# Performance work log

Hardware: AMD Instinct MI355X
Metric: run time of the kernel (lower is better)

Reference implementation:

```python
import jax, jax.numpy as jnp
import numpy as np

B, E, S = 4, 128, 4096


def setup_inputs() -> dict:
    key = jax.random.key(0)
    ks = jax.random.split(key, 7)
    x = jax.random.normal(ks[0], (B, E, S), dtype=jnp.float32)
    sd = 1.0 / np.sqrt(E)
    Wq = jax.random.normal(ks[1], (E, E), dtype=jnp.float32) * sd
    bq = jax.random.normal(ks[2], (E,), dtype=jnp.float32) * sd
    Wk = jax.random.normal(ks[3], (E, E), dtype=jnp.float32) * sd
    bk = jax.random.normal(ks[4], (E,), dtype=jnp.float32) * sd
    Wv = jax.random.normal(ks[5], (E, E), dtype=jnp.float32) * sd
    bv = jax.random.normal(ks[6], (E,), dtype=jnp.float32) * sd
    return {"x": x, "Wq": Wq, "bq": bq, "Wk": Wk, "bk": bk, "Wv": Wv, "bv": bv}


def reference(x, Wq, bq, Wk, bk, Wv, bv):
    # x: [B, E, S] -> [B, S, E] (matches x.transpose(1, 2) in the source)
    xt = jnp.swapaxes(x, 1, 2)
    # torch nn.Linear convention: y = x @ W.T + b
    q = xt @ Wq.T + bq  # [B, S, E]
    k = xt @ Wk.T + bk  # [B, S, E]
    v = xt @ Wv.T + bv  # [B, S, E]
    scale = 1.0 / jnp.sqrt(jnp.asarray(q.shape[-1], q.dtype))
    # full score matrix [B, S, S] -> softmax -> weighted sum of V
    scores = jax.nn.softmax(jnp.einsum("bse,bte->bst", q, k) * scale, axis=-1)
    out = jnp.einsum("bst,bte->bse", scores, v)  # [B, S, E]
    return out
```

## Files before the change

### kernel.cpp

```cpp
#include <hip/hip_runtime.h>

#define B_ 4
#define E_ 128
#define S_ 4096

typedef _Float16 half8 __attribute__((ext_vector_type(8)));
typedef _Float16 half4v __attribute__((ext_vector_type(4)));
typedef float floatx4 __attribute__((ext_vector_type(4)));

#define KQS (0.088388347648318447f * 1.4426950408889634f)

__device__ __forceinline__ floatx4 mfma16(half8 a, half8 b, floatx4 c) {
    return __builtin_amdgcn_mfma_f32_16x16x32_f16(a, b, c, 0, 0, 0);
}

__device__ __forceinline__ void gl_lds16(const void* g, void* l) {
    __builtin_amdgcn_global_load_lds(
        (const __attribute__((address_space(1))) void*)g,
        (__attribute__((address_space(3))) void*)l, 16, 0, 0);
}

__global__ void prep_w(const float* __restrict__ Wq, const float* __restrict__ Wk,
                       const float* __restrict__ Wv, _Float16* __restrict__ Wh) {
    int i = blockIdx.x * 256 + threadIdx.x;
    int mat = i >> 14;
    int j = i & 16383;
    float v = (mat == 0) ? Wq[j] * KQS : ((mat == 1) ? Wk[j] : Wv[j]);
    Wh[i] = (_Float16)v;
}

__global__ __launch_bounds__(256, 2) void proj(
    const float* __restrict__ x, const _Float16* __restrict__ Wh,
    const float* __restrict__ bq, const float* __restrict__ bk, const float* __restrict__ bv,
    _Float16* __restrict__ Qh, _Float16* __restrict__ Kh, _Float16* __restrict__ Vt) {
    __shared__ __align__(16) _Float16 sx[64 * 136];
    __shared__ __align__(16) _Float16 sk[64 * 136];
    __shared__ __align__(16) _Float16 sv[128 * 72];

    const int bid = blockIdx.x;
    const int b = bid >> 6;
    const int s0 = (bid & 63) << 6;
    const int tid = threadIdx.x;
    const int w = tid >> 6, lane = tid & 63;
    const int c = lane & 15, q = lane >> 4;

    const float* xb = x + (size_t)b * E_ * S_;
#pragma unroll
    for (int k = 0; k < 32; ++k) {
        int idx = k * 256 + tid;
        int e = idx >> 6, s = idx & 63;
        sx[s * 136 + e] = (_Float16)xb[e * S_ + s0 + s];
    }
    __syncthreads();

    half8 xf[4];
#pragma unroll
    for (int ch = 0; ch < 4; ++ch)
        xf[ch] = *(const half8*)&sx[(w * 16 + c) * 136 + ch * 32 + q * 8];
    __syncthreads();

    for (int eot = 0; eot < 8; ++eot) {
        half8 wf[3][4];
#pragma unroll
        for (int m = 0; m < 3; ++m)
#pragma unroll
            for (int ch = 0; ch < 4; ++ch)
                wf[m][ch] = *(const half8*)(Wh + ((m * E_ + eot * 16 + c) * E_ + ch * 32 + q * 8));

        floatx4 aq, ak, av;
        float bqv = bq[eot * 16 + c] * KQS;
        float bkv = bk[eot * 16 + c];
#pragma unroll
        for (int i = 0; i < 4; ++i) {
            aq[i] = bqv; ak[i] = bkv; av[i] = bv[eot * 16 + q * 4 + i];
        }
#pragma unroll
        for (int ch = 0; ch < 4; ++ch) {
            aq = mfma16(xf[ch], wf[0][ch], aq);
            ak = mfma16(xf[ch], wf[1][ch], ak);
            av = mfma16(wf[2][ch], xf[ch], av);
        }
#pragma unroll
        for (int i = 0; i < 4; ++i) {
            sx[(w * 16 + q * 4 + i) * 136 + eot * 16 + c] = (_Float16)aq[i];
            sk[(w * 16 + q * 4 + i) * 136 + eot * 16 + c] = (_Float16)ak[i];
            sv[(eot * 16 + q * 4 + i) * 72 + w * 16 + c] = (_Float16)av[i];
        }
    }
    __syncthreads();

#pragma unroll
    for (int p = 0; p < 4; ++p) {
        int idx = p * 256 + tid;
        int row = idx >> 4, chk = idx & 15;
        *(half8*)(Qh + ((size_t)(b * S_) + s0 + row) * E_ + chk * 8) =
            *(const half8*)&sx[row * 136 + chk * 8];
        *(half8*)(Kh + ((size_t)(b * S_) + s0 + row) * E_ + chk * 8) =
            *(const half8*)&sk[row * 136 + chk * 8];
        int vrow = idx >> 3, vch = idx & 7;
        *(half8*)(Vt + ((size_t)b * E_ + vrow) * S_ + s0 + vch * 8) =
            *(const half8*)&sv[vrow * 72 + vch * 8];
    }
}

__global__ __launch_bounds__(256, 2) void flash_attn(
    const _Float16* __restrict__ Qh, const _Float16* __restrict__ Kh,
    const _Float16* __restrict__ Vt, _Float16* __restrict__ Opart,
    float* __restrict__ lsum) {
    __shared__ __align__(16) _Float16 smem[32768];

    const int bid = blockIdx.x;
    const int b = bid >> 7, rem = bid & 127, qt = rem >> 2, part = rem & 3;
    const int tid = threadIdx.x, w = tid >> 6, lane = tid & 63;
    const int c = lane & 15, q = lane >> 4;

    const _Float16* Kb = Kh + ((size_t)b * S_ + part * 1024) * E_;
    const _Float16* Vb = Vt + (size_t)b * E_ * S_ + part * 1024;

    half8 qf[2][4];
    {
        const _Float16* Qb = Qh + ((size_t)b * S_ + qt * 128 + w * 32 + c) * E_;
#pragma unroll
        for (int st = 0; st < 2; ++st)
#pragma unroll
            for (int ch = 0; ch < 4; ++ch)
                qf[st][ch] = *(const half8*)(Qb + st * 16 * E_ + ch * 32 + q * 8);
    }

    floatx4 o[2][8];
    float lacc[2] = {0.f, 0.f};
#pragma unroll
    for (int st = 0; st < 2; ++st)
#pragma unroll
        for (int et = 0; et < 8; ++et) o[st][et] = (floatx4){0.f, 0.f, 0.f, 0.f};

    auto stageK = [&](int kt, int bi) {
        _Float16* Kd = smem + bi * 8192;
#pragma unroll
        for (int r = 0; r < 4; ++r) {
            int row = w * 16 + r * 4 + q;
            int lb = c ^ (row & 15);
            gl_lds16(Kb + ((size_t)(kt * 64 + row)) * E_ + lb * 8, Kd + (w * 16 + r * 4) * E_);
        }
    };
    auto stageV = [&](int kt, int bi) {
        _Float16* Vd = smem + 16384 + bi * 8192;
#pragma unroll
        for (int r = 0; r < 4; ++r) {
            int row = w * 32 + r * 8 + (lane >> 3);
            int lb = (lane & 7) ^ (row & 7);
            gl_lds16(Vb + (size_t)row * S_ + kt * 64 + lb * 8, Vd + (w * 32 + r * 8) * 64);
        }
    };

    stageK(0, 0); stageV(0, 0);
    for (int kt = 0; kt < 16; ++kt) {
        __syncthreads();
        if (kt + 1 < 16) { stageK(kt + 1, (kt + 1) & 1); stageV(kt + 1, (kt + 1) & 1); }

        const _Float16* K0 = smem + (kt & 1) * 8192;
        const _Float16* V0 = smem + 16384 + (kt & 1) * 8192;

        floatx4 sa[2][4];
#pragma unroll
        for (int st = 0; st < 2; ++st)
#pragma unroll
            for (int nt = 0; nt < 4; ++nt) sa[st][nt] = (floatx4){0.f, 0.f, 0.f, 0.f};
#pragma unroll
        for (int nt = 0; nt < 4; ++nt) {
            int row = nt * 16 + c;
#pragma unroll
            for (int ch = 0; ch < 4; ++ch) {
                int blk = (ch * 4 + q) ^ (row & 15);
                half8 kf = *(const half8*)(K0 + row * E_ + blk * 8);
                sa[0][nt] = mfma16(kf, qf[0][ch], sa[0][nt]);
                sa[1][nt] = mfma16(kf, qf[1][ch], sa[1][nt]);
            }
        }

        half8 pf[2][2];
#pragma unroll
        for (int st = 0; st < 2; ++st) {
#pragma unroll
            for (int nt = 0; nt < 4; ++nt) {
#pragma unroll
                for (int i = 0; i < 4; ++i) sa[st][nt][i] = exp2f(sa[st][nt][i]);
                lacc[st] += (sa[st][nt][0] + sa[st][nt][1]) + (sa[st][nt][2] + sa[st][nt][3]);
            }
#pragma unroll
            for (int ch = 0; ch < 2; ++ch) {
                half8 f;
#pragma unroll
                for (int j = 0; j < 8; ++j)
                    f[j] = (_Float16)sa[st][ch * 2 + (j >> 2)][j & 3];
                pf[st][ch] = f;
            }
        }

#pragma unroll
        for (int et = 0; et < 8; ++et) {
            int e = et * 16 + c;
            int sw = e & 7;
#pragma unroll
            for (int ch = 0; ch < 2; ++ch) {
                half4v lo = *(const half4v*)(V0 + e * 64 + (((ch * 4 + (q >> 1)) ^ sw) << 3) + (q & 1) * 4);
                half4v hi = *(const half4v*)(V0 + e * 64 + (((ch * 4 + 2 + (q >> 1)) ^ sw) << 3) + (q & 1) * 4);
                half8 vf = {lo[0], lo[1], lo[2], lo[3], hi[0], hi[1], hi[2], hi[3]};
                o[0][et] = mfma16(pf[0][ch], vf, o[0][et]);
                o[1][et] = mfma16(pf[1][ch], vf, o[1][et]);
            }
        }
    }
    __syncthreads();

#pragma unroll
    for (int st = 0; st < 2; ++st) {
        lacc[st] += __shfl_xor(lacc[st], 16);
        lacc[st] += __shfl_xor(lacc[st], 32);
    }
    if (q == 0) {
#pragma unroll
        for (int st = 0; st < 2; ++st)
            lsum[(size_t)bid * 128 + w * 32 + st * 16 + c] = lacc[st];
    }

    _Float16* Ot = smem + w * (32 * 136);
#pragma unroll
    for (int st = 0; st < 2; ++st) {
        float linv[4];
#pragma unroll
        for (int i = 0; i < 4; ++i) linv[i] = 1.0f / __shfl(lacc[st], q * 4 + i);
#pragma unroll
        for (int et = 0; et < 8; ++et)
#pragma unroll
            for (int i = 0; i < 4; ++i)
                Ot[(st * 16 + q * 4 + i) * 136 + et * 16 + c] = (_Float16)(o[st][et][i] * linv[i]);
    }
    __syncthreads();
    _Float16* OG = Opart + (size_t)bid * 16384;
#pragma unroll
    for (int p = 0; p < 8; ++p) {
        int idx = p * 64 + lane;
        int row = idx >> 4, chk = idx & 15;
        *(half8*)(OG + (w * 32 + row) * 128 + chk * 8) = *(const half8*)(Ot + row * 136 + chk * 8);
    }
}

__global__ void combine(const _Float16* __restrict__ Opart, const float* __restrict__ lsum,
                        float* __restrict__ out) {
    int t = blockIdx.x * 256 + threadIdx.x;
    int e4 = t & 31;
    int row = t >> 5;
    int b = row >> 12, s = row & 4095;
    int qt = s >> 7, r = s & 127;
    int bid0 = b * 128 + qt * 4;

    float l0 = lsum[(size_t)(bid0 + 0) * 128 + r];
    float l1 = lsum[(size_t)(bid0 + 1) * 128 + r];
    float l2 = lsum[(size_t)(bid0 + 2) * 128 + r];
    float l3 = lsum[(size_t)(bid0 + 3) * 128 + r];
    float inv = 1.f / (l0 + l1 + l2 + l3);
    float w0 = l0 * inv, w1 = l1 * inv, w2 = l2 * inv, w3 = l3 * inv;

    half4v n0 = *(const half4v*)(Opart + (size_t)(bid0 + 0) * 16384 + r * 128 + e4 * 4);
    half4v n1 = *(const half4v*)(Opart + (size_t)(bid0 + 1) * 16384 + r * 128 + e4 * 4);
    half4v n2 = *(const half4v*)(Opart + (size_t)(bid0 + 2) * 16384 + r * 128 + e4 * 4);
    half4v n3 = *(const half4v*)(Opart + (size_t)(bid0 + 3) * 16384 + r * 128 + e4 * 4);
    floatx4 res;
#pragma unroll
    for (int j = 0; j < 4; ++j)
        res[j] = (float)n0[j] * w0 + (float)n1[j] * w1 + (float)n2[j] * w2 + (float)n3[j] * w3;
    *(floatx4*)(out + (size_t)row * 128 + e4 * 4) = res;
}

extern "C" void kernel_launch(void* const* d_in, const int* in_sizes, int n_in,
                              void* d_out, int out_size, void* d_ws, size_t ws_size,
                              hipStream_t stream) {
    const float* x  = (const float*)d_in[0];
    const float* Wq = (const float*)d_in[1];
    const float* bq = (const float*)d_in[2];
    const float* Wk = (const float*)d_in[3];
    const float* bk = (const float*)d_in[4];
    const float* Wv = (const float*)d_in[5];
    const float* bv = (const float*)d_in[6];
    float* out = (float*)d_out;

    char* p = (char*)d_ws;
    _Float16* Wh = (_Float16*)p;
    _Float16* Qh = (_Float16*)(p + (1 << 17));
    _Float16* Kh = (_Float16*)(p + (1 << 17) + (1 << 22));
    _Float16* Vt = (_Float16*)(p + (1 << 17) + (2 << 22));
    _Float16* Op = (_Float16*)(p + (1 << 17) + (3 << 22));
    float* lsp   = (float*)(p + (1 << 17) + (3 << 22) + (1 << 24));

    prep_w<<<192, 256, 0, stream>>>(Wq, Wk, Wv, Wh);
    proj<<<256, 256, 0, stream>>>(x, Wh, bq, bk, bv, Qh, Kh, Vt);
    flash_attn<<<512, 256, 0, stream>>>(Qh, Kh, Vt, Op, lsp);
    combine<<<2048, 256, 0, stream>>>(Op, lsp, out);
}
```

Before: 141.8 us.

## Switch attention to 32x32x16 MFMA with 256-row query tiles and 8-way KV split

Rewrites the flash attention kernel to use 32x32x16 MFMA tiles, with each wave handling 64 query rows over a 512-key split (8 parts instead of 4). The projection kernel permutes V columns so the P fragments from the 32x32 accumulator layout line up with the V operand. Exp2 and fp16 packing move to raw builtins (exp2 and packed round-toward-zero convert). The aim is higher MFMA throughput and fewer LDS reads per flop, paid for with larger partial outputs, more combine traffic and higher register pressure.

```diff
diff --git a/kernel.cpp b/kernel.cpp
--- a/kernel.cpp
+++ b/kernel.cpp
@@ -6,12 +6,17 @@
 
 typedef _Float16 half8 __attribute__((ext_vector_type(8)));
 typedef _Float16 half4v __attribute__((ext_vector_type(4)));
+typedef __fp16 fp16x2 __attribute__((ext_vector_type(2)));
 typedef float floatx4 __attribute__((ext_vector_type(4)));
+typedef float floatx16 __attribute__((ext_vector_type(16)));
 
 #define KQS (0.088388347648318447f * 1.4426950408889634f)
 
 __device__ __forceinline__ floatx4 mfma16(half8 a, half8 b, floatx4 c) {
     return __builtin_amdgcn_mfma_f32_16x16x32_f16(a, b, c, 0, 0, 0);
+}
+__device__ __forceinline__ floatx16 mfma32(half8 a, half8 b, floatx16 c) {
+    return __builtin_amdgcn_mfma_f32_32x32x16_f16(a, b, c, 0, 0, 0);
 }
 
 __device__ __forceinline__ void gl_lds16(const void* g, void* l) {
@@ -43,6 +48,7 @@
     const int tid = threadIdx.x;
     const int w = tid >> 6, lane = tid & 63;
     const int c = lane & 15, q = lane >> 4;
+    const int pc = (c & 3) | (((c >> 3) & 1) << 2) | (((c >> 2) & 1) << 3);
 
     const float* xb = x + (size_t)b * E_ * S_;
 #pragma unroll
@@ -84,7 +90,7 @@
         for (int i = 0; i < 4; ++i) {
             sx[(w * 16 + q * 4 + i) * 136 + eot * 16 + c] = (_Float16)aq[i];
             sk[(w * 16 + q * 4 + i) * 136 + eot * 16 + c] = (_Float16)ak[i];
-            sv[(eot * 16 + q * 4 + i) * 72 + w * 16 + c] = (_Float16)av[i];
+            sv[(eot * 16 + q * 4 + i) * 72 + w * 16 + pc] = (_Float16)av[i];
         }
     }
     __syncthreads();
@@ -110,167 +116,161 @@
     __shared__ __align__(16) _Float16 smem[32768];
 
     const int bid = blockIdx.x;
-    const int b = bid >> 7, rem = bid & 127, qt = rem >> 2, part = rem & 3;
-    const int tid = threadIdx.x, w = tid >> 6, lane = tid & 63;
-    const int c = lane & 15, q = lane >> 4;
-
-    const _Float16* Kb = Kh + ((size_t)b * S_ + part * 1024) * E_;
-    const _Float16* Vb = Vt + (size_t)b * E_ * S_ + part * 1024;
-
-    half8 qf[2][4];
+    const int b = bid >> 7, rem = bid & 127, qt = rem >> 3, part = rem & 7;
+    const int tid = threadIdx.x, w = tid >> 6, l = tid & 63;
+    const int e5 = l & 31, hi = l >> 5;
+    const int c3 = (l >> 1) & 7;
+    const int c2 = (l >> 1) & 3;
+    const int b0 = (hi ^ l) & 1;
+
+    const _Float16* Kb = Kh + ((size_t)b * S_ + part * 512) * E_;
+    const _Float16* Vb = Vt + (size_t)b * E_ * S_ + part * 512;
+
+    half8 qf[2][8];
     {
-        const _Float16* Qb = Qh + ((size_t)b * S_ + qt * 128 + w * 32 + c) * E_;
-#pragma unroll
-        for (int st = 0; st < 2; ++st)
-#pragma unroll
-            for (int ch = 0; ch < 4; ++ch)
-                qf[st][ch] = *(const half8*)(Qb + st * 16 * E_ + ch * 32 + q * 8);
-    }
-
-    floatx4 o[2][8];
+        const _Float16* Qbase = Qh + ((size_t)b * S_ + qt * 256 + w * 64) * E_;
+#pragma unroll
+        for (int qb = 0; qb < 2; ++qb)
+#pragma unroll
+            for (int ech = 0; ech < 8; ++ech)
+                qf[qb][ech] = *(const half8*)(Qbase + (size_t)(qb * 32 + e5) * E_ + ech * 16 + hi * 8);
+    }
+
+    floatx16 o[2][4];
+#pragma unroll
+    for (int qb = 0; qb < 2; ++qb)
+#pragma unroll
+        for (int eb = 0; eb < 4; ++eb)
+#pragma unroll
+            for (int r = 0; r < 16; ++r) o[qb][eb][r] = 0.f;
     float lacc[2] = {0.f, 0.f};
-#pragma unroll
-    for (int st = 0; st < 2; ++st)
-#pragma unroll
-        for (int et = 0; et < 8; ++et) o[st][et] = (floatx4){0.f, 0.f, 0.f, 0.f};
-
-    auto stageK = [&](int kt, int bi) {
+
+    auto stage = [&](int kt, int bi) {
         _Float16* Kd = smem + bi * 8192;
 #pragma unroll
         for (int r = 0; r < 4; ++r) {
-            int row = w * 16 + r * 4 + q;
-            int lb = c ^ (row & 15);
-            gl_lds16(Kb + ((size_t)(kt * 64 + row)) * E_ + lb * 8, Kd + (w * 16 + r * 4) * E_);
+            int krow = w * 16 + r * 4 + (l >> 4);
+            gl_lds16(Kb + (size_t)(kt * 64 + krow) * E_ + (((l & 15) ^ (r * 4 + (l >> 4))) * 8),
+                     Kd + (w * 16 + r * 4) * 128);
+        }
+        _Float16* Vd = smem + 16384 + bi * 8192;
+#pragma unroll
+        for (int r = 0; r < 4; ++r) {
+            int vrow = w * 32 + r * 8 + (l >> 3);
+            gl_lds16(Vb + (size_t)vrow * S_ + kt * 64 + (((l & 7) ^ (l >> 3)) * 8),
+                     Vd + (w * 32 + r * 8) * 64);
         }
     };
-    auto stageV = [&](int kt, int bi) {
-        _Float16* Vd = smem + 16384 + bi * 8192;
-#pragma unroll
-        for (int r = 0; r < 4; ++r) {
-            int row = w * 32 + r * 8 + (lane >> 3);
-            int lb = (lane & 7) ^ (row & 7);
-            gl_lds16(Vb + (size_t)row * S_ + kt * 64 + lb * 8, Vd + (w * 32 + r * 8) * 64);
-        }
-    };
-
-    stageK(0, 0); stageV(0, 0);
-    for (int kt = 0; kt < 16; ++kt) {
+
+    stage(0, 0);
+    for (int kt = 0; kt < 8; ++kt) {
         __syncthreads();
-        if (kt + 1 < 16) { stageK(kt + 1, (kt + 1) & 1); stageV(kt + 1, (kt + 1) & 1); }
-
+        if (kt < 7) stage(kt + 1, (kt + 1) & 1);
         const _Float16* K0 = smem + (kt & 1) * 8192;
         const _Float16* V0 = smem + 16384 + (kt & 1) * 8192;
 
-        floatx4 sa[2][4];
-#pragma unroll
-        for (int st = 0; st < 2; ++st)
-#pragma unroll
-            for (int nt = 0; nt < 4; ++nt) sa[st][nt] = (floatx4){0.f, 0.f, 0.f, 0.f};
-#pragma unroll
-        for (int nt = 0; nt < 4; ++nt) {
-            int row = nt * 16 + c;
-#pragma unroll
-            for (int ch = 0; ch < 4; ++ch) {
-                int blk = (ch * 4 + q) ^ (row & 15);
-                half8 kf = *(const half8*)(K0 + row * E_ + blk * 8);
-                sa[0][nt] = mfma16(kf, qf[0][ch], sa[0][nt]);
-                sa[1][nt] = mfma16(kf, qf[1][ch], sa[1][nt]);
+        half8 pf[2][4];
+#pragma unroll
+        for (int kvb = 0; kvb < 2; ++kvb) {
+            floatx16 s0, s1;
+#pragma unroll
+            for (int r = 0; r < 16; ++r) { s0[r] = 0.f; s1[r] = 0.f; }
+#pragma unroll
+            for (int ech = 0; ech < 8; ++ech) {
+                const half8 kf = *(const half8*)(K0 + (kvb * 32 + e5) * 128 +
+                                                 ((((ech ^ c3) << 1) | b0) * 8));
+                s0 = mfma32(kf, qf[0][ech], s0);
+                s1 = mfma32(kf, qf[1][ech], s1);
             }
-        }
-
-        half8 pf[2][2];
-#pragma unroll
-        for (int st = 0; st < 2; ++st) {
-#pragma unroll
-            for (int nt = 0; nt < 4; ++nt) {
-#pragma unroll
-                for (int i = 0; i < 4; ++i) sa[st][nt][i] = exp2f(sa[st][nt][i]);
-                lacc[st] += (sa[st][nt][0] + sa[st][nt][1]) + (sa[st][nt][2] + sa[st][nt][3]);
+#pragma unroll
+            for (int h = 0; h < 2; ++h) {
+                float p0[8], p1[8];
+#pragma unroll
+                for (int j = 0; j < 8; ++j) {
+                    p0[j] = __builtin_amdgcn_exp2f(s0[h * 8 + j]);
+                    p1[j] = __builtin_amdgcn_exp2f(s1[h * 8 + j]);
+                }
+#pragma unroll
+                for (int j = 0; j < 8; ++j) { lacc[0] += p0[j]; lacc[1] += p1[j]; }
+                union { half8 h8; fp16x2 h2[4]; } u0, u1;
+#pragma unroll
+                for (int k2 = 0; k2 < 4; ++k2) {
+                    u0.h2[k2] = __builtin_amdgcn_cvt_pkrtz(p0[2 * k2], p0[2 * k2 + 1]);
+                    u1.h2[k2] = __builtin_amdgcn_cvt_pkrtz(p1[2 * k2], p1[2 * k2 + 1]);
+                }
+                pf[0][kvb * 2 + h] = u0.h8;
+                pf[1][kvb * 2 + h] = u1.h8;
             }
-#pragma unroll
-            for (int ch = 0; ch < 2; ++ch) {
-                half8 f;
-#pragma unroll
-                for (int j = 0; j < 8; ++j)
-                    f[j] = (_Float16)sa[st][ch * 2 + (j >> 2)][j & 3];
-                pf[st][ch] = f;
+        }
+
+#pragma unroll
+        for (int eb = 0; eb < 4; ++eb) {
+#pragma unroll
+            for (int t = 0; t < 4; ++t) {
+                const half8 vf = *(const half8*)(V0 + (eb * 32 + e5) * 64 +
+                                                 ((((t ^ c2) << 1) | b0) * 8));
+                o[0][eb] = mfma32(pf[0][t], vf, o[0][eb]);
+                o[1][eb] = mfma32(pf[1][t], vf, o[1][eb]);
             }
         }
-
-#pragma unroll
-        for (int et = 0; et < 8; ++et) {
-            int e = et * 16 + c;
-            int sw = e & 7;
-#pragma unroll
-            for (int ch = 0; ch < 2; ++ch) {
-                half4v lo = *(const half4v*)(V0 + e * 64 + (((ch * 4 + (q >> 1)) ^ sw) << 3) + (q & 1) * 4);
-                half4v hi = *(const half4v*)(V0 + e * 64 + (((ch * 4 + 2 + (q >> 1)) ^ sw) << 3) + (q & 1) * 4);
-                half8 vf = {lo[0], lo[1], lo[2], lo[3], hi[0], hi[1], hi[2], hi[3]};
-                o[0][et] = mfma16(pf[0][ch], vf, o[0][et]);
-                o[1][et] = mfma16(pf[1][ch], vf, o[1][et]);
-            }
-        }
-    }
+    }
+
+#pragma unroll
+    for (int qb = 0; qb < 2; ++qb) lacc[qb] += __shfl_xor(lacc[qb], 32);
+    if (hi == 0) {
+        lsum[(size_t)bid * 256 + w * 64 + e5] = lacc[0];
+        lsum[(size_t)bid * 256 + w * 64 + 32 + e5] = lacc[1];
+    }
+    float linv[2] = {1.f / lacc[0], 1.f / lacc[1]};
+
     __syncthreads();
-
-#pragma unroll
-    for (int st = 0; st < 2; ++st) {
-        lacc[st] += __shfl_xor(lacc[st], 16);
-        lacc[st] += __shfl_xor(lacc[st], 32);
-    }
-    if (q == 0) {
-#pragma unroll
-        for (int st = 0; st < 2; ++st)
-            lsum[(size_t)bid * 128 + w * 32 + st * 16 + c] = lacc[st];
-    }
-
-    _Float16* Ot = smem + w * (32 * 136);
-#pragma unroll
-    for (int st = 0; st < 2; ++st) {
-        float linv[4];
-#pragma unroll
-        for (int i = 0; i < 4; ++i) linv[i] = 1.0f / __shfl(lacc[st], q * 4 + i);
-#pragma unroll
-        for (int et = 0; et < 8; ++et)
-#pragma unroll
-            for (int i = 0; i < 4; ++i)
-                Ot[(st * 16 + q * 4 + i) * 136 + et * 16 + c] = (_Float16)(o[st][et][i] * linv[i]);
-    }
-    __syncthreads();
-    _Float16* OG = Opart + (size_t)bid * 16384;
-#pragma unroll
-    for (int p = 0; p < 8; ++p) {
-        int idx = p * 64 + lane;
-        int row = idx >> 4, chk = idx & 15;
-        *(half8*)(OG + (w * 32 + row) * 128 + chk * 8) = *(const half8*)(Ot + row * 136 + chk * 8);
+    _Float16* Ot = smem + w * 8192;
+#pragma unroll
+    for (int qb = 0; qb < 2; ++qb)
+#pragma unroll
+        for (int r = 0; r < 16; ++r) {
+            int rl = (r & 3) + 8 * (r >> 2) + 4 * hi;
+            float s = __shfl(linv[qb], rl);
+            int row = qb * 32 + rl;
+#pragma unroll
+            for (int eb = 0; eb < 4; ++eb)
+                Ot[row * 128 + eb * 32 + e5] = (_Float16)(o[qb][eb][r] * s);
+        }
+    _Float16* OG = Opart + (size_t)bid * 32768 + w * 8192;
+#pragma unroll
+    for (int p4 = 0; p4 < 16; ++p4) {
+        int idx = p4 * 64 + l;
+        *(half8*)(OG + idx * 8) = *(const half8*)(Ot + idx * 8);
     }
 }
 
 __global__ void combine(const _Float16* __restrict__ Opart, const float* __restrict__ lsum,
                         float* __restrict__ out) {
     int t = blockIdx.x * 256 + threadIdx.x;
-    int e4 = t & 31;
-    int row = t >> 5;
+    int e8 = t & 15;
+    int row = t >> 4;
     int b = row >> 12, s = row & 4095;
-    int qt = s >> 7, r = s & 127;
-    int bid0 = b * 128 + qt * 4;
-
-    float l0 = lsum[(size_t)(bid0 + 0) * 128 + r];
-    float l1 = lsum[(size_t)(bid0 + 1) * 128 + r];
-    float l2 = lsum[(size_t)(bid0 + 2) * 128 + r];
-    float l3 = lsum[(size_t)(bid0 + 3) * 128 + r];
-    float inv = 1.f / (l0 + l1 + l2 + l3);
-    float w0 = l0 * inv, w1 = l1 * inv, w2 = l2 * inv, w3 = l3 * inv;
-
-    half4v n0 = *(const half4v*)(Opart + (size_t)(bid0 + 0) * 16384 + r * 128 + e4 * 4);
-    half4v n1 = *(const half4v*)(Opart + (size_t)(bid0 + 1) * 16384 + r * 128 + e4 * 4);
-    half4v n2 = *(const half4v*)(Opart + (size_t)(bid0 + 2) * 16384 + r * 128 + e4 * 4);
-    half4v n3 = *(const half4v*)(Opart + (size_t)(bid0 + 3) * 16384 + r * 128 + e4 * 4);
-    floatx4 res;
-#pragma unroll
-    for (int j = 0; j < 4; ++j)
-        res[j] = (float)n0[j] * w0 + (float)n1[j] * w1 + (float)n2[j] * w2 + (float)n3[j] * w3;
-    *(floatx4*)(out + (size_t)row * 128 + e4 * 4) = res;
+    int qt = s >> 8, r = s & 255;
+    int base = b * 128 + qt * 8;
+
+    float lv[8], tot = 0.f;
+#pragma unroll
+    for (int p = 0; p < 8; ++p) { lv[p] = lsum[(size_t)(base + p) * 256 + r]; tot += lv[p]; }
+    float inv = 1.f / tot;
+
+    float acc[8];
+#pragma unroll
+    for (int j = 0; j < 8; ++j) acc[j] = 0.f;
+#pragma unroll
+    for (int p = 0; p < 8; ++p) {
+        half8 n = *(const half8*)(Opart + (size_t)(base + p) * 32768 + r * 128 + e8 * 8);
+        float wp = lv[p] * inv;
+#pragma unroll
+        for (int j = 0; j < 8; ++j) acc[j] += (float)n[j] * wp;
+    }
+    float* op = out + (size_t)row * 128 + e8 * 8;
+    *(floatx4*)op = (floatx4){acc[0], acc[1], acc[2], acc[3]};
+    *(floatx4*)(op + 4) = (floatx4){acc[4], acc[5], acc[6], acc[7]};
 }
 
 extern "C" void kernel_launch(void* const* d_in, const int* in_sizes, int n_in,
@@ -291,10 +291,10 @@
     _Float16* Kh = (_Float16*)(p + (1 << 17) + (1 << 22));
     _Float16* Vt = (_Float16*)(p + (1 << 17) + (2 << 22));
     _Float16* Op = (_Float16*)(p + (1 << 17) + (3 << 22));
-    float* lsp   = (float*)(p + (1 << 17) + (3 << 22) + (1 << 24));
+    float* lsp   = (float*)(p + (1 << 17) + (3 << 22) + (1 << 25));
 
     prep_w<<<192, 256, 0, stream>>>(Wq, Wk, Wv, Wh);
     proj<<<256, 256, 0, stream>>>(x, Wh, bq, bk, bv, Qh, Kh, Vt);
     flash_attn<<<512, 256, 0, stream>>>(Qh, Kh, Vt, Op, lsp);
-    combine<<<2048, 256, 0, stream>>>(Op, lsp, out);
-}
+    combine<<<1024, 256, 0, stream>>>(Op, lsp, out);
+}
```

New measurement: 198.9 us. +40.2%, slower.
